# Kernel optimization log

Hardware: AMD Instinct MI355X
Metric: run time of the kernel (lower is better)

Reference implementation:

```python
import jax, jax.numpy as jnp
import numpy as np

BATCH, SEQ_LEN, D_MODEL, STATE_N, N_CLASSES = 32, 4096, 256, 64, 5


def setup_inputs() -> dict:
    key = jax.random.key(0)
    ks = jax.random.split(key, 9)
    x = jax.random.normal(ks[0], (BATCH, SEQ_LEN), jnp.float32)
    w_in = jax.random.normal(ks[1], (D_MODEL,), jnp.float32)
    b_in = jax.random.normal(ks[2], (D_MODEL,), jnp.float32) * 0.1
    # stable diagonal transition in (0.9, 0.999)
    A_diag = 0.9 + 0.099 * jax.random.uniform(ks[3], (D_MODEL, STATE_N), jnp.float32)
    B_in = jax.random.normal(ks[4], (D_MODEL, STATE_N), jnp.float32) * 0.1
    C_out = jax.random.normal(ks[5], (D_MODEL, STATE_N), jnp.float32) * 0.1
    D_skip = jax.random.normal(ks[6], (D_MODEL,), jnp.float32)
    W_head = jax.random.normal(ks[7], (2 * D_MODEL, N_CLASSES), jnp.float32) * 0.05
    b_head = jnp.zeros((N_CLASSES,), jnp.float32)
    return {"x": x, "w_in": w_in, "b_in": b_in, "A_diag": A_diag, "B_in": B_in,
            "C_out": C_out, "D_skip": D_skip, "W_head": W_head, "b_head": b_head}


def reference(x, w_in, b_in, A_diag, B_in, C_out, D_skip, W_head, b_head):
    # x: [B, T] scalar ECG signal; diagonal SSM recurrence over T via lax.scan
    Bsz = x.shape[0]
    D, N = A_diag.shape

    def step(s, xt):
        # xt: [B] scalar input at time t; project to channels
        u = xt[:, None] * w_in + b_in              # [B, D]
        s = A_diag * s + B_in * u[:, :, None]      # [B, D, N]
        h = jax.nn.gelu(jnp.einsum('bdn,dn->bd', s, C_out) + D_skip * u)  # [B, D]
        return s, h

    s0 = jnp.zeros((Bsz, D, N), x.dtype)
    _, h_all = jax.lax.scan(step, s0, x.T)         # h_all: [T, B, D]
    avg_p = h_all.mean(axis=0)                     # [B, D]
    max_p = h_all.max(axis=0)                      # [B, D]
    pooled = jnp.concatenate([avg_p, max_p], axis=-1)  # [B, 2D] (streaming_pool='avgmax')
    return pooled @ W_head + b_head                # [B, n_classes]
```

## Files before the change

### kernel.cpp

```cpp
#include <hip/hip_runtime.h>

#define BATCH 32
#define SEQ 4096
#define DMODEL 256
#define NCLS 5

typedef short          s8v __attribute__((ext_vector_type(8)));
typedef unsigned short u8v __attribute__((ext_vector_type(8)));
typedef float          f4v __attribute__((ext_vector_type(4)));

__device__ __forceinline__ unsigned short f2b(float f) {
    unsigned u = __float_as_uint(f);
    u += 0x7FFFu + ((u >> 16) & 1u);
    return (unsigned short)(u >> 16);
}

__global__ __launch_bounds__(512) void ssm_mfma_kernel(
    const float* __restrict__ x,
    const float* __restrict__ w_in,
    const float* __restrict__ b_in,
    const float* __restrict__ A_diag,
    const float* __restrict__ B_in,
    const float* __restrict__ C_out,
    const float* __restrict__ D_skip,
    const float* __restrict__ W_head,
    const float* __restrict__ b_head,
    float* __restrict__ out)
{
    __shared__ __align__(16) unsigned char smem[71936];
    float*          XAf  = (float*)smem;
    unsigned short* Xb   = (unsigned short*)(smem + 34816);
    unsigned short* Sigb = (unsigned short*)(smem + 53248);
    float*          Pow  = (float*)smem;
    unsigned short* MAb  = (unsigned short*)(smem + 16640);
    unsigned short* CATb = (unsigned short*)(smem + 25856);
    unsigned short* TGb  = (unsigned short*)(smem + 35072);
    float* A64f = (float*)(smem + 44288);
    float* cQf  = (float*)(smem + 44544);
    float* Pf   = (float*)(smem + 44800);
    float* Qf   = (float*)(smem + 45056);
    float* Gf   = (float*)(smem + 45312);
    float* Hf   = (float*)(smem + 45568);
    float* Hcp  = (float*)(smem + 71680);
    float* ps   = (float*)smem;
    float* pm   = (float*)(smem + 512);

    const int tid  = threadIdx.x;
    const int lane = tid & 63;
    const int wid  = tid >> 6;
    const int m16  = lane & 15;
    const int q4   = (lane >> 4) * 4;
    const int q8   = (lane >> 4) * 8;
    const int cb   = wid * 16;
    const int d    = blockIdx.x >> 1;
    const int bh   = blockIdx.x & 1;

    const float wd = w_in[d], bd = b_in[d];
    const float Dw = D_skip[d] * wd;
    const float Db = D_skip[d] * bd;

    if (tid < 64) {
        const int n = tid;
        const float An = A_diag[d * 64 + n];
        const float CB = B_in[d * 64 + n] * C_out[d * 64 + n];
        const float Pn = CB * wd, Qn = CB * bd;
        Pf[n] = Pn; Qf[n] = Qn;
        float p = 1.0f, a64 = 1.0f;
        for (int m = 0; m < 65; ++m) { Pow[m * 64 + n] = p; a64 = p; p *= An; }
        A64f[n] = a64;
        cQf[n]  = Qn * (1.0f - a64) / (1.0f - An);
    }
    __syncthreads();
    {
        const int r0 = tid >> 3, c0 = (tid & 7) * 8;
        #pragma unroll
        for (int jj = 0; jj < 8; ++jj) {
            const int j = c0 + jj;
            MAb [r0 * 72 + j] = f2b(Pow[(63 - j) * 64 + r0]);
            CATb[r0 * 72 + j] = f2b(Pow[(r0 + 1) * 64 + j]);
        }
        if (tid < 64) {
            float g = 0.0f, h = 0.0f;
            for (int nn = 0; nn < 64; ++nn) {
                const float pw = Pow[tid * 64 + nn];
                g = fmaf(pw, Pf[nn], g);
                h = fmaf(pw, Qf[nn], h);
            }
            Gf[tid] = g; Hf[tid] = h;
        }
    }
    __syncthreads();
    {
        const int k0 = tid >> 3, c0 = (tid & 7) * 8;
        #pragma unroll
        for (int jj = 0; jj < 8; ++jj) {
            const int j = c0 + jj;
            TGb[k0 * 72 + j] = (j < k0)  ? f2b(Gf[k0 - j])
                             : (j == k0) ? f2b(Gf[0] + Dw)
                                         : (unsigned short)0;
        }
        if (tid < 64) {
            float a = Db;
            for (int m = 0; m <= tid; ++m) a += Hf[m];
            Hcp[tid] = a;
        }
    }
    __syncthreads();

    s8v aMA[4][2], aCAT[4][2], aTG[4][2];
    #pragma unroll
    for (int rt = 0; rt < 4; ++rt)
        #pragma unroll
        for (int kb = 0; kb < 2; ++kb) {
            const int off = (rt * 16 + m16) * 72 + kb * 32 + q8;
            aMA [rt][kb] = *(const s8v*)&MAb [off];
            aCAT[rt][kb] = *(const s8v*)&CATb[off];
            aTG [rt][kb] = *(const s8v*)&TGb [off];
        }
    const int   n2   = (tid & 31) * 2;
    const int   bC   = tid >> 5;
    const float a64x = A64f[n2], a64y = A64f[n2 + 1];
    const float Px   = Pf[n2],   Py   = Pf[n2 + 1];
    const float cQx  = cQf[n2],  cQy  = cQf[n2 + 1];
    __syncthreads();

    const int colA = tid >> 2;
    const int j0A  = (tid & 3) * 16;
    const int cA   = colA >> 4, blA = colA & 15;
    const float* xrow = x + (bh * 16 + blA) * SEQ + cA * 64 + j0A;
    unsigned short* xdst = &Xb[colA * 72 + j0A];

    float sx = 0.0f, sy = 0.0f;
    float psum = 0.0f, pmax = -1e30f;

    for (int g = 0; g < 8; ++g) {
        const float4* xg = (const float4*)(xrow + g * 512);
        const float4 u0 = xg[0], u1 = xg[1], u2 = xg[2], u3 = xg[3];
        u8v lo, hi;
        lo[0]=f2b(u0.x); lo[1]=f2b(u0.y); lo[2]=f2b(u0.z); lo[3]=f2b(u0.w);
        lo[4]=f2b(u1.x); lo[5]=f2b(u1.y); lo[6]=f2b(u1.z); lo[7]=f2b(u1.w);
        hi[0]=f2b(u2.x); hi[1]=f2b(u2.y); hi[2]=f2b(u2.z); hi[3]=f2b(u2.w);
        hi[4]=f2b(u3.x); hi[5]=f2b(u3.y); hi[6]=f2b(u3.z); hi[7]=f2b(u3.w);
        *(u8v*)(xdst)     = lo;
        *(u8v*)(xdst + 8) = hi;
        __syncthreads();

        const s8v bx0 = *(const s8v*)&Xb[(cb + m16) * 72 + q8];
        const s8v bx1 = *(const s8v*)&Xb[(cb + m16) * 72 + 32 + q8];
        #pragma unroll
        for (int rt = 0; rt < 4; ++rt) {
            f4v acc = {0.0f, 0.0f, 0.0f, 0.0f};
            acc = __builtin_amdgcn_mfma_f32_16x16x32_bf16(aMA[rt][0], bx0, acc, 0, 0, 0);
            acc = __builtin_amdgcn_mfma_f32_16x16x32_bf16(aMA[rt][1], bx1, acc, 0, 0, 0);
            *(f4v*)&XAf[(cb + m16) * 68 + rt * 16 + q4] = acc;
        }
        __syncthreads();

        #pragma unroll
        for (int c = 0; c < 8; ++c) {
            const int col = c * 16 + bC;
            *(unsigned*)&Sigb[col * 72 + n2] =
                ((unsigned)f2b(sy) << 16) | (unsigned)f2b(sx);
            const float2 xa = *(const float2*)&XAf[col * 68 + n2];
            sx = fmaf(a64x, sx, fmaf(Px, xa.x, cQx));
            sy = fmaf(a64y, sy, fmaf(Py, xa.y, cQy));
        }
        __syncthreads();

        const s8v bs0 = *(const s8v*)&Sigb[(cb + m16) * 72 + q8];
        const s8v bs1 = *(const s8v*)&Sigb[(cb + m16) * 72 + 32 + q8];
        #pragma unroll
        for (int rt = 0; rt < 4; ++rt) {
            f4v acc = {0.0f, 0.0f, 0.0f, 0.0f};
            acc = __builtin_amdgcn_mfma_f32_16x16x32_bf16(aCAT[rt][0], bs0, acc, 0, 0, 0);
            acc = __builtin_amdgcn_mfma_f32_16x16x32_bf16(aCAT[rt][1], bs1, acc, 0, 0, 0);
            acc = __builtin_amdgcn_mfma_f32_16x16x32_bf16(aTG [rt][0], bx0, acc, 0, 0, 0);
            acc = __builtin_amdgcn_mfma_f32_16x16x32_bf16(aTG [rt][1], bx1, acc, 0, 0, 0);
            #pragma unroll
            for (int r = 0; r < 4; ++r) {
                const float yt = acc[r] + Hcp[rt * 16 + q4 + r];
                const float y2 = yt * yt;
                const float zn = yt * fmaf(-0.07135481627f, y2, -1.5957691216f);
                const float h  = yt * __builtin_amdgcn_rcpf(1.0f + __expf(zn));
                psum += h;
                pmax = fmaxf(pmax, h);
            }
        }
        __syncthreads();
    }

    psum += __shfl_xor(psum, 16, 64); psum += __shfl_xor(psum, 32, 64);
    pmax = fmaxf(pmax, __shfl_xor(pmax, 16, 64));
    pmax = fmaxf(pmax, __shfl_xor(pmax, 32, 64));
    if (lane < 16) {
        ps[wid * 16 + lane] = psum;
        pm[wid * 16 + lane] = pmax;
    }
    __syncthreads();
    if (tid < 16) {
        float s = 0.0f, m = -1e30f;
        #pragma unroll
        for (int w = 0; w < 8; ++w) {
            s += ps[w * 16 + tid];
            m = fmaxf(m, pm[w * 16 + tid]);
        }
        s *= (1.0f / SEQ);
        const int b = bh * 16 + tid;
        #pragma unroll
        for (int c = 0; c < NCLS; ++c) {
            const float v = fmaf(s, W_head[d * NCLS + c],
                                 m * W_head[(DMODEL + d) * NCLS + c]);
            unsafeAtomicAdd(&out[b * NCLS + c], v);
        }
    }
    if (blockIdx.x < 2 && tid < 80)
        unsafeAtomicAdd(&out[bh * 80 + tid], b_head[tid % NCLS]);
}

extern "C" void kernel_launch(void* const* d_in, const int* in_sizes, int n_in,
                              void* d_out, int out_size, void* d_ws, size_t ws_size,
                              hipStream_t stream) {
    const float* x      = (const float*)d_in[0];
    const float* w_in   = (const float*)d_in[1];
    const float* b_in   = (const float*)d_in[2];
    const float* A_diag = (const float*)d_in[3];
    const float* B_in   = (const float*)d_in[4];
    const float* C_out  = (const float*)d_in[5];
    const float* D_skip = (const float*)d_in[6];
    const float* W_head = (const float*)d_in[7];
    const float* b_head = (const float*)d_in[8];
    float* out = (float*)d_out;
    ssm_mfma_kernel<<<2 * DMODEL, 512, 0, stream>>>(
        x, w_in, b_in, A_diag, B_in, C_out, D_skip, W_head, b_head, out);
}
```

Baseline: 133.0 us.

## Give each wavefront private batch rows to replace block barriers with LDS fences

```diff
diff --git a/kernel.cpp b/kernel.cpp
--- a/kernel.cpp
+++ b/kernel.cpp
@@ -14,6 +14,8 @@
     u += 0x7FFFu + ((u >> 16) & 1u);
     return (unsigned short)(u >> 16);
 }
+
+#define LDS_FENCE() asm volatile("s_waitcnt lgkmcnt(0)" ::: "memory")
 
 __global__ __launch_bounds__(512) void ssm_mfma_kernel(
     const float* __restrict__ x,
@@ -27,10 +29,7 @@
     const float* __restrict__ b_head,
     float* __restrict__ out)
 {
-    __shared__ __align__(16) unsigned char smem[71936];
-    float*          XAf  = (float*)smem;
-    unsigned short* Xb   = (unsigned short*)(smem + 34816);
-    unsigned short* Sigb = (unsigned short*)(smem + 53248);
+    __shared__ __align__(16) unsigned char smem[73984];
     float*          Pow  = (float*)smem;
     unsigned short* MAb  = (unsigned short*)(smem + 16640);
     unsigned short* CATb = (unsigned short*)(smem + 25856);
@@ -41,19 +40,30 @@
     float* Qf   = (float*)(smem + 45056);
     float* Gf   = (float*)(smem + 45312);
     float* Hf   = (float*)(smem + 45568);
-    float* Hcp  = (float*)(smem + 71680);
-    float* ps   = (float*)smem;
-    float* pm   = (float*)(smem + 512);
+    float* Hcp  = (float*)(smem + 73728);
 
     const int tid  = threadIdx.x;
     const int lane = tid & 63;
     const int wid  = tid >> 6;
     const int m16  = lane & 15;
-    const int q4   = (lane >> 4) * 4;
-    const int q8   = (lane >> 4) * 8;
-    const int cb   = wid * 16;
+    const int q    = lane >> 4;
+    const int q4   = q * 4;
+    const int q8   = q * 8;
     const int d    = blockIdx.x >> 1;
     const int bh   = blockIdx.x & 1;
+
+    unsigned short* Xb_w  = (unsigned short*)(smem + wid * 9216);
+    float*          XAf_w = (float*)(smem + wid * 9216 + 2304);
+    unsigned short* Sig_w = (unsigned short*)(smem + wid * 9216 + 6912);
+
+    const int cA = m16 & 7;
+    const int bl = m16 >> 3;
+    const int gb = bh * 16 + wid * 2 + bl;
+    const float* xlane = x + gb * SEQ + cA * 64 + q * 16;
+    float4 p0 = ((const float4*)xlane)[0];
+    float4 p1 = ((const float4*)xlane)[1];
+    float4 p2 = ((const float4*)xlane)[2];
+    float4 p3 = ((const float4*)xlane)[3];
 
     const float wd = w_in[d], bd = b_in[d];
     const float Dw = D_skip[d] * wd;
@@ -117,68 +127,68 @@
             aCAT[rt][kb] = *(const s8v*)&CATb[off];
             aTG [rt][kb] = *(const s8v*)&TGb [off];
         }
-    const int   n2   = (tid & 31) * 2;
-    const int   bC   = tid >> 5;
+    const int   sb   = lane >> 5;
+    const int   n2   = (lane & 31) * 2;
     const float a64x = A64f[n2], a64y = A64f[n2 + 1];
     const float Px   = Pf[n2],   Py   = Pf[n2 + 1];
     const float cQx  = cQf[n2],  cQy  = cQf[n2 + 1];
     __syncthreads();
 
-    const int colA = tid >> 2;
-    const int j0A  = (tid & 3) * 16;
-    const int cA   = colA >> 4, blA = colA & 15;
-    const float* xrow = x + (bh * 16 + blA) * SEQ + cA * 64 + j0A;
-    unsigned short* xdst = &Xb[colA * 72 + j0A];
-
     float sx = 0.0f, sy = 0.0f;
     float psum = 0.0f, pmax = -1e30f;
 
+    #pragma unroll 1
     for (int g = 0; g < 8; ++g) {
-        const float4* xg = (const float4*)(xrow + g * 512);
-        const float4 u0 = xg[0], u1 = xg[1], u2 = xg[2], u3 = xg[3];
         u8v lo, hi;
-        lo[0]=f2b(u0.x); lo[1]=f2b(u0.y); lo[2]=f2b(u0.z); lo[3]=f2b(u0.w);
-        lo[4]=f2b(u1.x); lo[5]=f2b(u1.y); lo[6]=f2b(u1.z); lo[7]=f2b(u1.w);
-        hi[0]=f2b(u2.x); hi[1]=f2b(u2.y); hi[2]=f2b(u2.z); hi[3]=f2b(u2.w);
-        hi[4]=f2b(u3.x); hi[5]=f2b(u3.y); hi[6]=f2b(u3.z); hi[7]=f2b(u3.w);
-        *(u8v*)(xdst)     = lo;
-        *(u8v*)(xdst + 8) = hi;
-        __syncthreads();
-
-        const s8v bx0 = *(const s8v*)&Xb[(cb + m16) * 72 + q8];
-        const s8v bx1 = *(const s8v*)&Xb[(cb + m16) * 72 + 32 + q8];
+        lo[0]=f2b(p0.x); lo[1]=f2b(p0.y); lo[2]=f2b(p0.z); lo[3]=f2b(p0.w);
+        lo[4]=f2b(p1.x); lo[5]=f2b(p1.y); lo[6]=f2b(p1.z); lo[7]=f2b(p1.w);
+        hi[0]=f2b(p2.x); hi[1]=f2b(p2.y); hi[2]=f2b(p2.z); hi[3]=f2b(p2.w);
+        hi[4]=f2b(p3.x); hi[5]=f2b(p3.y); hi[6]=f2b(p3.z); hi[7]=f2b(p3.w);
+        *(u8v*)&Xb_w[m16 * 72 + q * 16]     = lo;
+        *(u8v*)&Xb_w[m16 * 72 + q * 16 + 8] = hi;
+        if (g < 7) {
+            const float4* xn = (const float4*)(xlane + (g + 1) * 512);
+            p0 = xn[0]; p1 = xn[1]; p2 = xn[2]; p3 = xn[3];
+        }
+        LDS_FENCE();
+
+        const s8v bx0 = *(const s8v*)&Xb_w[m16 * 72 + q8];
+        const s8v bx1 = *(const s8v*)&Xb_w[m16 * 72 + 32 + q8];
+        f4v acc[4];
         #pragma unroll
         for (int rt = 0; rt < 4; ++rt) {
-            f4v acc = {0.0f, 0.0f, 0.0f, 0.0f};
-            acc = __builtin_amdgcn_mfma_f32_16x16x32_bf16(aMA[rt][0], bx0, acc, 0, 0, 0);
-            acc = __builtin_amdgcn_mfma_f32_16x16x32_bf16(aMA[rt][1], bx1, acc, 0, 0, 0);
-            *(f4v*)&XAf[(cb + m16) * 68 + rt * 16 + q4] = acc;
-        }
-        __syncthreads();
-
+            f4v a0 = {0.0f, 0.0f, 0.0f, 0.0f};
+            a0 = __builtin_amdgcn_mfma_f32_16x16x32_bf16(aMA[rt][0], bx0, a0, 0, 0, 0);
+            acc[rt] = __builtin_amdgcn_mfma_f32_16x16x32_bf16(aMA[rt][1], bx1, a0, 0, 0, 0);
+        }
+        #pragma unroll
+        for (int rt = 0; rt < 4; ++rt)
+            *(f4v*)&XAf_w[m16 * 72 + rt * 16 + q4] = acc[rt];
+        LDS_FENCE();
         #pragma unroll
         for (int c = 0; c < 8; ++c) {
-            const int col = c * 16 + bC;
-            *(unsigned*)&Sigb[col * 72 + n2] =
+            const int col = sb * 8 + c;
+            *(unsigned*)&Sig_w[col * 72 + n2] =
                 ((unsigned)f2b(sy) << 16) | (unsigned)f2b(sx);
-            const float2 xa = *(const float2*)&XAf[col * 68 + n2];
+            const float2 xa = *(const float2*)&XAf_w[col * 72 + n2];
             sx = fmaf(a64x, sx, fmaf(Px, xa.x, cQx));
             sy = fmaf(a64y, sy, fmaf(Py, xa.y, cQy));
         }
-        __syncthreads();
-
-        const s8v bs0 = *(const s8v*)&Sigb[(cb + m16) * 72 + q8];
-        const s8v bs1 = *(const s8v*)&Sigb[(cb + m16) * 72 + 32 + q8];
+        LDS_FENCE();
+
+        const s8v bs0 = *(const s8v*)&Sig_w[m16 * 72 + q8];
+        const s8v bs1 = *(const s8v*)&Sig_w[m16 * 72 + 32 + q8];
         #pragma unroll
         for (int rt = 0; rt < 4; ++rt) {
-            f4v acc = {0.0f, 0.0f, 0.0f, 0.0f};
-            acc = __builtin_amdgcn_mfma_f32_16x16x32_bf16(aCAT[rt][0], bs0, acc, 0, 0, 0);
-            acc = __builtin_amdgcn_mfma_f32_16x16x32_bf16(aCAT[rt][1], bs1, acc, 0, 0, 0);
-            acc = __builtin_amdgcn_mfma_f32_16x16x32_bf16(aTG [rt][0], bx0, acc, 0, 0, 0);
-            acc = __builtin_amdgcn_mfma_f32_16x16x32_bf16(aTG [rt][1], bx1, acc, 0, 0, 0);
+            f4v a2 = {0.0f, 0.0f, 0.0f, 0.0f};
+            a2 = __builtin_amdgcn_mfma_f32_16x16x32_bf16(aCAT[rt][0], bs0, a2, 0, 0, 0);
+            a2 = __builtin_amdgcn_mfma_f32_16x16x32_bf16(aCAT[rt][1], bs1, a2, 0, 0, 0);
+            a2 = __builtin_amdgcn_mfma_f32_16x16x32_bf16(aTG [rt][0], bx0, a2, 0, 0, 0);
+            a2 = __builtin_amdgcn_mfma_f32_16x16x32_bf16(aTG [rt][1], bx1, a2, 0, 0, 0);
+            const f4v hv = *(const f4v*)&Hcp[rt * 16 + q4];
             #pragma unroll
             for (int r = 0; r < 4; ++r) {
-                const float yt = acc[r] + Hcp[rt * 16 + q4 + r];
+                const float yt = a2[r] + hv[r];
                 const float y2 = yt * yt;
                 const float zn = yt * fmaf(-0.07135481627f, y2, -1.5957691216f);
                 const float h  = yt * __builtin_amdgcn_rcpf(1.0f + __expf(zn));
@@ -186,30 +196,23 @@
                 pmax = fmaxf(pmax, h);
             }
         }
-        __syncthreads();
     }
 
     psum += __shfl_xor(psum, 16, 64); psum += __shfl_xor(psum, 32, 64);
     pmax = fmaxf(pmax, __shfl_xor(pmax, 16, 64));
     pmax = fmaxf(pmax, __shfl_xor(pmax, 32, 64));
-    if (lane < 16) {
-        ps[wid * 16 + lane] = psum;
-        pm[wid * 16 + lane] = pmax;
-    }
-    __syncthreads();
-    if (tid < 16) {
-        float s = 0.0f, m = -1e30f;
-        #pragma unroll
-        for (int w = 0; w < 8; ++w) {
-            s += ps[w * 16 + tid];
-            m = fmaxf(m, pm[w * 16 + tid]);
-        }
-        s *= (1.0f / SEQ);
-        const int b = bh * 16 + tid;
+    #pragma unroll
+    for (int off = 1; off <= 4; off <<= 1) {
+        psum += __shfl_xor(psum, off, 64);
+        pmax = fmaxf(pmax, __shfl_xor(pmax, off, 64));
+    }
+    if ((lane & 55) == 0) {
+        const int b = bh * 16 + wid * 2 + (lane >> 3);
+        const float s = psum * (1.0f / SEQ);
         #pragma unroll
         for (int c = 0; c < NCLS; ++c) {
             const float v = fmaf(s, W_head[d * NCLS + c],
-                                 m * W_head[(DMODEL + d) * NCLS + c]);
+                                 pmax * W_head[(DMODEL + d) * NCLS + c]);
             unsafeAtomicAdd(&out[b * NCLS + c], v);
         }
     }
```

After: 155.2 us. +16.7%, slower.
